# Optimization experiments

Measured on AMD Instinct MI355X. Metric: run time of the kernel, lower is better.

Reference implementation:

```python
import jax, jax.numpy as jnp
import numpy as np

D_MODEL = 256
NUM_HEADS = 8
CHUNK = 500
KEY_DIM = D_MODEL // NUM_HEADS      # 32
HEAD_DIM = KEY_DIM                  # value_factor = 1
SCALING = KEY_DIM ** -0.5
B, C, T = 2, 4, 2000                # T must be a multiple of CHUNK


def _rel_pos_constants(slen):
    # RetNetRelPos(chunkwise_recurrent=True)
    angle = 1.0 / (10000.0 ** jnp.linspace(0.0, 1.0, KEY_DIM // 2))
    angle = jnp.repeat(angle, 2)                                     # (KEY_DIM,)
    decay = jnp.log(1.0 - 2.0 ** (-5.0 - jnp.arange(NUM_HEADS, dtype=jnp.float32)))
    idx = jnp.arange(slen, dtype=jnp.float32)
    sin = jnp.sin(idx[:, None] * angle[None, :])                     # (T, KEY_DIM)
    cos = jnp.cos(idx[:, None] * angle[None, :])
    bi = jnp.arange(CHUNK, dtype=jnp.float32)
    diff = bi[:, None] - bi[None, :]
    mask = jnp.where(diff >= 0, jnp.exp(decay[:, None, None] * diff), 0.0)  # (H, cs, cs)
    last_row_sum = mask[:, -1].sum(-1)                               # (H,)
    value_inner_decay = (mask[:, -1] / last_row_sum[:, None])[:, :, None]   # (H, cs, 1)
    scale = jnp.sqrt(mask.sum(-1, keepdims=True))                    # (H, cs, 1)
    inner_mask = mask / scale
    cross_decay = jnp.exp(decay * CHUNK)[:, None, None]              # (H, 1, 1)
    qid = jnp.exp(decay[:, None] * (bi + 1.0))[:, :, None]           # (H, cs, 1)
    query_inner_decay = qid / (scale / last_row_sum[:, None, None])
    return sin, cos, inner_mask, cross_decay, query_inner_decay, value_inner_decay


def _rotate_every_two(x):
    x1, x2 = x[..., ::2], x[..., 1::2]
    return jnp.stack((-x2, x1), axis=-1).reshape(x.shape)


def _theta_shift(x, sin, cos):
    return x * cos + _rotate_every_two(x) * sin


def _layer_norm(x, g, b, eps=1e-5):
    mu = x.mean(-1, keepdims=True)
    var = ((x - mu) ** 2).mean(-1, keepdims=True)
    return (x - mu) * jax.lax.rsqrt(var + eps) * g + b


def _retention(x, qw, kw, vw, gw, ow):
    # MultiScaleRetention, chunkwise-recurrent mode
    bsz, t, _ = x.shape
    sin, cos, mask, cross_decay, q_decay, v_decay = _rel_pos_constants(t)
    q = x @ qw.T
    k = (x @ kw.T) * SCALING
    v = x @ vw.T
    g = x @ gw.T
    q = q.reshape(bsz, t, NUM_HEADS, KEY_DIM).transpose(0, 2, 1, 3)
    k = k.reshape(bsz, t, NUM_HEADS, KEY_DIM).transpose(0, 2, 1, 3)
    qr = _theta_shift(q, sin, cos)
    kr = _theta_shift(k, sin, cos)
    nc = t // CHUNK
    qr = qr.reshape(bsz, NUM_HEADS, nc, CHUNK, KEY_DIM).transpose(0, 2, 1, 3, 4)
    kr = kr.reshape(bsz, NUM_HEADS, nc, CHUNK, KEY_DIM).transpose(0, 2, 1, 3, 4)
    v = v.reshape(bsz, nc, CHUNK, NUM_HEADS, HEAD_DIM).transpose(0, 1, 3, 2, 4)
    qk = jnp.einsum('bnhik,bnhjk->bnhij', qr, kr) * mask             # (b,nc,h,cs,cs)
    inner_scale = jnp.maximum(jax.lax.stop_gradient(jnp.abs(qk)).sum(-1, keepdims=True), 1.0)
    inner_out = (qk / inner_scale) @ v                               # (b,nc,h,cs,hd)
    kv = jnp.einsum('bnhjk,bnhjd->bnhkd', kr, v * v_decay)           # (b,nc,h,kd,hd)

    def step(carry, kv_i):
        kv_state, kv_scale = carry
        out = (kv_state / kv_scale, kv_scale)
        kv_state = kv_state * cross_decay + kv_i
        kv_scale = jnp.maximum(
            jax.lax.stop_gradient(jnp.abs(kv_state)).sum(-2, keepdims=True).max(-1, keepdims=True), 1.0)
        return (kv_state, kv_scale), out

    init = (jnp.zeros((bsz, NUM_HEADS, KEY_DIM, HEAD_DIM), v.dtype),
            jnp.ones((bsz, NUM_HEADS, 1, 1), v.dtype))
    _, (kv_rec, cross_scale) = jax.lax.scan(step, init, jnp.moveaxis(kv, 1, 0))
    kv_rec = jnp.moveaxis(kv_rec, 0, 1)                              # (b,nc,h,kd,hd)
    cross_scale = jnp.moveaxis(cross_scale, 0, 1)                    # (b,nc,h,1,1)
    all_scale = jnp.maximum(inner_scale, cross_scale)
    cross_out = jnp.einsum('bnhik,bnhkd->bnhid', qr * q_decay, kv_rec)
    out = inner_out / (all_scale / inner_scale) + cross_out / (all_scale / cross_scale)
    out = out.transpose(0, 1, 3, 2, 4)                               # (b,nc,cs,h,hd)
    # group_norm = RMSNorm(head_dim, eps=1e-6, no affine)
    out = out * jax.lax.rsqrt(jnp.mean(out ** 2, -1, keepdims=True) + 1e-6)
    out = out.reshape(bsz, t, NUM_HEADS * HEAD_DIM)
    return (jax.nn.silu(g) * out) @ ow.T


def _mha(x, in_w, in_b, out_w, out_b):
    # torch.nn.MultiheadAttention, batch_first, eval (dropout off)
    bsz, s, _ = x.shape
    hd = D_MODEL // NUM_HEADS
    qkv = x @ in_w.T + in_b
    q, k, v = jnp.split(qkv, 3, axis=-1)
    q = q.reshape(bsz, s, NUM_HEADS, hd).transpose(0, 2, 1, 3) * (hd ** -0.5)
    k = k.reshape(bsz, s, NUM_HEADS, hd).transpose(0, 2, 1, 3)
    v = v.reshape(bsz, s, NUM_HEADS, hd).transpose(0, 2, 1, 3)
    attn = jax.nn.softmax(jnp.einsum('bhqd,bhkd->bhqk', q, k), axis=-1)
    out = jnp.einsum('bhqk,bhkd->bhqd', attn, v).transpose(0, 2, 1, 3).reshape(bsz, s, D_MODEL)
    return out @ out_w.T + out_b


def setup_inputs() -> dict:
    key = jax.random.key(0)
    ks = jax.random.split(key, 10)
    s = D_MODEL ** -0.5
    return {
        'inputs': jax.random.normal(ks[0], (B, C, T, D_MODEL), jnp.float32),
        'ln1_g': jnp.ones((D_MODEL,), jnp.float32),
        'ln1_b': jnp.zeros((D_MODEL,), jnp.float32),
        'ln2_g': jnp.ones((D_MODEL,), jnp.float32),
        'ln2_b': jnp.zeros((D_MODEL,), jnp.float32),
        'qw': jax.random.normal(ks[1], (D_MODEL, D_MODEL), jnp.float32) * s,
        'kw': jax.random.normal(ks[2], (D_MODEL, D_MODEL), jnp.float32) * s,
        'vw': jax.random.normal(ks[3], (D_MODEL, D_MODEL), jnp.float32) * s,
        'gw': jax.random.normal(ks[4], (D_MODEL, D_MODEL), jnp.float32) * s,
        'ow': jax.random.normal(ks[5], (D_MODEL, D_MODEL), jnp.float32) * s,
        'in_w': jax.random.normal(ks[6], (3 * D_MODEL, D_MODEL), jnp.float32) * s,
        'in_b': jnp.zeros((3 * D_MODEL,), jnp.float32),
        'out_w': jax.random.normal(ks[7], (D_MODEL, D_MODEL), jnp.float32) * s,
        'out_b': jnp.zeros((D_MODEL,), jnp.float32),
    }


def reference(inputs, ln1_g, ln1_b, ln2_g, ln2_b, qw, kw, vw, gw, ow, in_w, in_b, out_w, out_b):
    Bb, Cc, Tt, Dd = inputs.shape
    x = inputs.reshape(Bb * Cc, Tt, Dd)
    x = x + _retention(_layer_norm(x, ln1_g, ln1_b), qw, kw, vw, gw, ow)
    x = x.reshape(Bb, Cc, Tt, Dd).transpose(0, 2, 1, 3).reshape(Bb * Tt, Cc, Dd)
    x = x + _mha(_layer_norm(x, ln2_g, ln2_b), in_w, in_b, out_w, out_b)
    return x.reshape(Bb, Tt, Cc, Dd).transpose(0, 2, 1, 3)
```

## Files before the change

### kernel.cpp

```cpp
#include <hip/hip_runtime.h>
#include <math.h>

#define TLEN 2000
#define NSEQ 8
#define NHEADS 8
#define KD 32
#define CHUNKN 500
#define NCHUNK 4
#define MROWS 16000
#define SCALING 0.1767766952966369f

typedef float f32x4 __attribute__((ext_vector_type(4)));
typedef short s16x8 __attribute__((ext_vector_type(8)));
typedef unsigned short u16x8 __attribute__((ext_vector_type(8)));
typedef unsigned short u16x4 __attribute__((ext_vector_type(4)));

__device__ __forceinline__ unsigned short f2bf(float f) {
    unsigned int u = __float_as_uint(f);
    unsigned int r = (u + 0x7FFFu + ((u >> 16) & 1u)) >> 16;
    return (unsigned short)r;
}
__device__ __forceinline__ float bf2f(unsigned short h) {
    return __uint_as_float(((unsigned int)h) << 16);
}
__device__ __forceinline__ unsigned int cvtpk(float lo, float hi) {
    unsigned int r;
    asm("v_cvt_pk_bf16_f32 %0, %1, %2" : "=v"(r) : "v"(lo), "v"(hi));
    return r;
}

__global__ __launch_bounds__(256) void tab_kernel(float* __restrict__ sinT,
                                                  float* __restrict__ cosT) {
    int idx = blockIdx.x * 256 + threadIdx.x;
    if (idx >= TLEN * 16) return;
    int t = idx >> 4, a = idx & 15;
    float ang = powf(10000.0f, -(float)a / 15.0f);
    float th = (float)t * ang;
    sinT[idx] = sinf(th);
    cosT[idx] = cosf(th);
}

__global__ __launch_bounds__(256) void wcast_kernel(
    const float* __restrict__ qw, const float* __restrict__ kw,
    const float* __restrict__ vw, const float* __restrict__ gw,
    const float* __restrict__ ow, const float* __restrict__ inw,
    const float* __restrict__ outw, unsigned short* __restrict__ W) {
    int i = blockIdx.x * 1024 + threadIdx.x * 4;
    const float* src; int off;
    if (i < 65536)       { src = qw;   off = i; }
    else if (i < 131072) { src = kw;   off = i - 65536; }
    else if (i < 196608) { src = vw;   off = i - 131072; }
    else if (i < 262144) { src = gw;   off = i - 196608; }
    else if (i < 327680) { src = ow;   off = i - 262144; }
    else if (i < 524288) { src = inw;  off = i - 327680; }
    else                 { src = outw; off = i - 524288; }
    float4 v = *(const float4*)(src + off);
    u16x4 o;
    o[0] = f2bf(v.x); o[1] = f2bf(v.y); o[2] = f2bf(v.z); o[3] = f2bf(v.w);
    *(u16x4*)(W + i) = o;
}

__global__ __launch_bounds__(256) void ln_kernel(const float* __restrict__ x,
                                                 const float* __restrict__ gam,
                                                 const float* __restrict__ bet,
                                                 unsigned short* __restrict__ H,
                                                 unsigned short* __restrict__ L,
                                                 int rows) {
    int wid = threadIdx.x >> 6, lane = threadIdx.x & 63;
    int row = blockIdx.x * 4 + wid;
    if (row >= rows) return;
    const float* xr = x + (size_t)row * 256;
    float4 v = *(const float4*)(xr + lane * 4);
    float s = v.x + v.y + v.z + v.w;
    #pragma unroll
    for (int o = 32; o; o >>= 1) s += __shfl_xor(s, o);
    float mu = s * (1.0f / 256.0f);
    float dx = v.x - mu, dy = v.y - mu, dz = v.z - mu, dw = v.w - mu;
    float ss = dx * dx + dy * dy + dz * dz + dw * dw;
    #pragma unroll
    for (int o = 32; o; o >>= 1) ss += __shfl_xor(ss, o);
    float rstd = rsqrtf(ss * (1.0f / 256.0f) + 1e-5f);
    float4 g4 = *(const float4*)(gam + lane * 4);
    float4 b4 = *(const float4*)(bet + lane * 4);
    float ov[4];
    ov[0] = dx * rstd * g4.x + b4.x;
    ov[1] = dy * rstd * g4.y + b4.y;
    ov[2] = dz * rstd * g4.z + b4.z;
    ov[3] = dw * rstd * g4.w + b4.w;
    u16x4 hv, lv;
    #pragma unroll
    for (int j = 0; j < 4; ++j) {
        hv[j] = f2bf(ov[j]);
        lv[j] = f2bf(ov[j] - bf2f(hv[j]));
    }
    *(u16x4*)(H + (size_t)row * 256 + lane * 4) = hv;
    *(u16x4*)(L + (size_t)row * 256 + lane * 4) = lv;
}

template <int MODE>
__global__ __launch_bounds__(256, 2) void gemm_mfma(
    const unsigned short* __restrict__ AH, const unsigned short* __restrict__ AL,
    const unsigned short* __restrict__ Wc, const float* __restrict__ sinT,
    const float* __restrict__ cosT, const float* __restrict__ bias,
    const float* __restrict__ resid, float* __restrict__ F0,
    unsigned short* __restrict__ U0, unsigned short* __restrict__ U1,
    unsigned short* __restrict__ U2, unsigned short* __restrict__ U3,
    unsigned short* __restrict__ U4) {
    __shared__ unsigned short Ah[128][72];
    __shared__ unsigned short Al[128][72];
    __shared__ unsigned short Bt[128][72];
    const int tid = threadIdx.x;
    const int m0 = blockIdx.y * 128, n0 = blockIdx.x * 128;
    size_t wbase;
    if constexpr (MODE == 0)      wbase = (size_t)(n0 >> 8) * 65536 + (size_t)(n0 & 255) * 256;
    else if constexpr (MODE == 1) wbase = 262144 + (size_t)n0 * 256;
    else if constexpr (MODE == 2) wbase = 327680 + (size_t)n0 * 256;
    else                          wbase = 524288 + (size_t)n0 * 256;

    const int wid = tid >> 6, lane = tid & 63;
    const int wm = wid >> 1, wn = wid & 1;
    const int lr = lane & 15, lk = lane >> 4;
    const int str = tid >> 3;
    const int stc = (tid & 7) * 8;

    f32x4 acc[4][4] = {};

    for (int kt = 0; kt < 256; kt += 64) {
        if (kt) __syncthreads();
        #pragma unroll
        for (int it = 0; it < 4; ++it) {
            int r = it * 32 + str;
            u16x8 va = *(const u16x8*)(AH + (size_t)(m0 + r) * 256 + kt + stc);
            u16x8 vl = *(const u16x8*)(AL + (size_t)(m0 + r) * 256 + kt + stc);
            u16x8 vw = *(const u16x8*)(Wc + wbase + (size_t)r * 256 + kt + stc);
            *(u16x8*)(&Ah[r][stc]) = va;
            *(u16x8*)(&Al[r][stc]) = vl;
            *(u16x8*)(&Bt[r][stc]) = vw;
        }
        __syncthreads();
        #pragma unroll
        for (int ks = 0; ks < 2; ++ks) {
            const int k0 = ks * 32 + lk * 8;
            s16x8 af[4], alf[4], bf[4];
            #pragma unroll
            for (int f = 0; f < 4; ++f) {
                af[f]  = *(const s16x8*)(&Ah[wm * 64 + f * 16 + lr][k0]);
                alf[f] = *(const s16x8*)(&Al[wm * 64 + f * 16 + lr][k0]);
                bf[f]  = *(const s16x8*)(&Bt[wn * 64 + f * 16 + lr][k0]);
            }
            #pragma unroll
            for (int fm = 0; fm < 4; ++fm)
                #pragma unroll
                for (int fn = 0; fn < 4; ++fn) {
                    acc[fm][fn] = __builtin_amdgcn_mfma_f32_16x16x32_bf16(af[fm], bf[fn], acc[fm][fn], 0, 0, 0);
                    acc[fm][fn] = __builtin_amdgcn_mfma_f32_16x16x32_bf16(alf[fm], bf[fn], acc[fm][fn], 0, 0, 0);
                }
        }
    }

    if constexpr (MODE == 0) {
        const int w = n0 >> 8;
        if (w <= 1) {
            const float sc = (w == 1) ? SCALING : 1.0f;
            #pragma unroll
            for (int fn = 0; fn < 4; ++fn) {
                const int c = n0 + wn * 64 + fn * 16 + lr;
                const int d0 = c & 31;
                #pragma unroll
                for (int fm = 0; fm < 4; ++fm)
                    #pragma unroll
                    for (int r = 0; r < 4; ++r) {
                        const int i = m0 + wm * 64 + fm * 16 + lk * 4 + r;
                        const int t = i % TLEN;
                        float vraw = acc[fm][fn][r] * sc;
                        float oth = __shfl_xor(vraw, 1);
                        float cs = cosT[t * 16 + (d0 >> 1)];
                        float sn = sinT[t * 16 + (d0 >> 1)];
                        acc[fm][fn][r] = (d0 & 1) ? fmaf(vraw, cs, oth * sn)
                                                  : fmaf(vraw, cs, -(oth * sn));
                    }
            }
        }
        unsigned short* Dsel = (w == 0) ? U0 : (w == 1) ? U2 : (w == 2) ? U3 : U4;
        for (int half = 0; half < 2; ++half) {
            const int np = (w == 0) ? 2 : 1;
            for (int pass = 0; pass < np; ++pass) {
                __syncthreads();
                if (wn == half) {
                    #pragma unroll
                    for (int fn = 0; fn < 4; ++fn)
                        #pragma unroll
                        for (int fm = 0; fm < 4; ++fm)
                            #pragma unroll
                            for (int r = 0; r < 4; ++r) {
                                float x = acc[fm][fn][r];
                                unsigned short hb = f2bf(x);
                                unsigned short ob = pass ? f2bf(x - bf2f(hb)) : hb;
                                Ah[wm * 64 + fm * 16 + lk * 4 + r][fn * 16 + lr] = ob;
                            }
                }
                __syncthreads();
                unsigned short* D = (w == 0 && pass) ? U1 : Dsel;
                #pragma unroll
                for (int it = 0; it < 4; ++it) {
                    int flat = it * 2048 + tid * 8;
                    int r = flat >> 6, cl = flat & 63;
                    u16x8 val = *(const u16x8*)&Ah[r][cl];
                    int i = m0 + r;
                    int cb = (n0 & 255) + half * 64 + cl;
                    if (w <= 2) {
                        int bb = i / TLEN, t = i - bb * TLEN;
                        int hh = cb >> 5, d0 = cb & 31;
                        *(u16x8*)(D + ((size_t)(bb * NHEADS + hh) * TLEN + t) * KD + d0) = val;
                    } else {
                        *(u16x8*)(D + (size_t)i * 256 + cb) = val;
                    }
                }
            }
        }
    } else if constexpr (MODE == 1) {
        #pragma unroll
        for (int fn = 0; fn < 4; ++fn) {
            const int c = n0 + wn * 64 + fn * 16 + lr;
            #pragma unroll
            for (int fm = 0; fm < 4; ++fm)
                #pragma unroll
                for (int r = 0; r < 4; ++r) {
                    const int i = m0 + wm * 64 + fm * 16 + lk * 4 + r;
                    F0[(size_t)i * 256 + c] = resid[(size_t)i * 256 + c] + acc[fm][fn][r];
                }
        }
    } else if constexpr (MODE == 2) {
        const int w = n0 >> 8;
        const float qs = (w == 0) ? SCALING : 1.0f;
        unsigned short* Dsel = (w == 0) ? U0 : (w == 1) ? U1 : U2;
        #pragma unroll
        for (int fn = 0; fn < 4; ++fn) {
            const int c = n0 + wn * 64 + fn * 16 + lr;
            const float bv = bias[c];
            #pragma unroll
            for (int fm = 0; fm < 4; ++fm)
                #pragma unroll
                for (int r = 0; r < 4; ++r)
                    acc[fm][fn][r] = (acc[fm][fn][r] + bv) * qs;
        }
        for (int half = 0; half < 2; ++half) {
            __syncthreads();
            if (wn == half) {
                #pragma unroll
                for (int fn = 0; fn < 4; ++fn)
                    #pragma unroll
                    for (int fm = 0; fm < 4; ++fm)
                        #pragma unroll
                        for (int r = 0; r < 4; ++r)
                            Ah[wm * 64 + fm * 16 + lk * 4 + r][fn * 16 + lr] =
                                f2bf(acc[fm][fn][r]);
            }
            __syncthreads();
            #pragma unroll
            for (int it = 0; it < 4; ++it) {
                int flat = it * 2048 + tid * 8;
                int r = flat >> 6, cl = flat & 63;
                u16x8 val = *(const u16x8*)&Ah[r][cl];
                int i = m0 + r;
                int cb = (n0 & 255) + half * 64 + cl;
                *(u16x8*)(Dsel + (size_t)i * 256 + cb) = val;
            }
        }
    } else {
        #pragma unroll
        for (int fn = 0; fn < 4; ++fn) {
            const int c = n0 + wn * 64 + fn * 16 + lr;
            const float bv = bias[c];
            #pragma unroll
            for (int fm = 0; fm < 4; ++fm)
                #pragma unroll
                for (int r = 0; r < 4; ++r) {
                    const int i = m0 + wm * 64 + fm * 16 + lk * 4 + r;
                    F0[(size_t)i * 256 + c] = resid[(size_t)i * 256 + c] + acc[fm][fn][r] + bv;
                }
        }
    }
}

__global__ __launch_bounds__(256) void kvp_kernel(const unsigned short* __restrict__ KB,
                                                  const unsigned short* __restrict__ VB,
                                                  float* __restrict__ kvp) {
    int blk = blockIdx.x;
    int sub = blk & 1, rest = blk >> 1;
    int b = rest >> 5, n = (rest >> 3) & 3, h = rest & 7;
    int tid = threadIdx.x;
    int k = tid >> 3, d0 = (tid & 7) * 4;
    float dec = logf(1.0f - exp2f(-5.0f - (float)h));
    float lrs = (1.0f - expf(dec * (float)CHUNKN)) / (1.0f - expf(dec));
    float invl = 1.0f / lrs;
    const unsigned short* krb = KB + ((size_t)(b * NHEADS + h) * TLEN + n * CHUNKN) * KD;
    const unsigned short* vb = VB + ((size_t)(b * NHEADS + h) * TLEN + n * CHUNKN) * KD;
    float a0 = 0, a1 = 0, a2 = 0, a3 = 0;
    int j0 = sub * 250;
    for (int j = j0; j < j0 + 250; ++j) {
        float kj = bf2f(krb[(size_t)j * KD + k]);
        float vd = expf(dec * (float)(CHUNKN - 1 - j)) * invl;
        float w = kj * vd;
        u16x4 vv = *(const u16x4*)(vb + (size_t)j * KD + d0);
        a0 = fmaf(w, bf2f(vv[0]), a0); a1 = fmaf(w, bf2f(vv[1]), a1);
        a2 = fmaf(w, bf2f(vv[2]), a2); a3 = fmaf(w, bf2f(vv[3]), a3);
    }
    float* dst = kvp + ((size_t)rest * 2 + sub) * 1024 + k * 32 + d0;
    dst[0] = a0; dst[1] = a1; dst[2] = a2; dst[3] = a3;
}

__global__ __launch_bounds__(256) void scan_kernel(const float* __restrict__ kvp,
                                                   float* __restrict__ rec,
                                                   float* __restrict__ sig) {
    __shared__ float cs[32];
    __shared__ float ssig;
    int blk = blockIdx.x;
    int b = blk >> 3, h = blk & 7;
    int tid = threadIdx.x;
    float dec = logf(1.0f - exp2f(-5.0f - (float)h));
    float cd = expf(dec * (float)CHUNKN);
    float S0 = 0, S1 = 0, S2 = 0, S3 = 0;
    float sigma = 1.0f;
    for (int n = 0; n < NCHUNK; ++n) {
        int rest = b * 32 + n * 8 + h;
        size_t rbase = (size_t)rest * 1024;
        size_t pbase = (size_t)rest * 2048;
        rec[rbase + tid] = S0;
        rec[rbase + tid + 256] = S1;
        rec[rbase + tid + 512] = S2;
        rec[rbase + tid + 768] = S3;
        if (tid == 0) sig[rest] = sigma;
        float k0 = 0, k1 = 0, k2 = 0, k3 = 0;
        #pragma unroll
        for (int s = 0; s < 2; ++s) {
            k0 += kvp[pbase + s * 1024 + tid];
            k1 += kvp[pbase + s * 1024 + tid + 256];
            k2 += kvp[pbase + s * 1024 + tid + 512];
            k3 += kvp[pbase + s * 1024 + tid + 768];
        }
        S0 = S0 * cd + k0;
        S1 = S1 * cd + k1;
        S2 = S2 * cd + k2;
        S3 = S3 * cd + k3;
        if (tid < 32) cs[tid] = 0.f;
        __syncthreads();
        float part = fabsf(S0) + fabsf(S1) + fabsf(S2) + fabsf(S3);
        atomicAdd(&cs[tid & 31], part);
        __syncthreads();
        if (tid == 0) {
            float m = cs[0];
            for (int d = 1; d < 32; ++d) m = fmaxf(m, cs[d]);
            ssig = fmaxf(m, 1.0f);
        }
        __syncthreads();
        sigma = ssig;
    }
}

__global__ __launch_bounds__(256, 2) void ret_core3(
    const unsigned short* __restrict__ QH, const unsigned short* __restrict__ QL,
    const unsigned short* __restrict__ KB, const unsigned short* __restrict__ VB,
    const unsigned short* __restrict__ GB,
    const float* __restrict__ rec, const float* __restrict__ sig,
    unsigned short* __restrict__ ABH, unsigned short* __restrict__ ABL) {
    __shared__ unsigned short Kt[64][40];
    __shared__ unsigned short Vt[32][72];
    __shared__ unsigned short SpH[32][40];
    __shared__ unsigned short SpL[32][40];
    __shared__ unsigned short Pl[128][72];

    const int u = 3 - (int)(blockIdx.x >> 8);
    const int chunk = blockIdx.x & 255;
    const int b = chunk >> 5, n = (chunk >> 3) & 3, h = chunk & 7;
    const int tid = threadIdx.x;
    const int wid = tid >> 6, lane = tid & 63;
    const int c = lane & 15, gq = lane >> 4;
    const float dec = logf(1.0f - exp2f(-5.0f - (float)h));
    const float ndec = -dec;
    const size_t cb16 = ((size_t)(b * NHEADS + h) * TLEN + n * CHUNKN) * KD;
    const int i0 = u * 128 + wid * 32;
    const int NT = 2 * u + 2;
    const int jtmax_w = (i0 + 31) >> 6;

    s16x8 qh[2], ql[2];
    #pragma unroll
    for (int fi = 0; fi < 2; ++fi) {
        size_t off = cb16 + (size_t)(i0 + fi * 16 + c) * KD + gq * 8;
        qh[fi] = *(const s16x8*)(QH + off);
        ql[fi] = *(const s16x8*)(QL + off);
    }

    {
        int e0 = tid * 4;
        int k = e0 >> 5, d0 = e0 & 31;
        float4 sv = *(const float4*)(rec + (size_t)chunk * 1024 + e0);
        float se[4] = {sv.x, sv.y, sv.z, sv.w};
        #pragma unroll
        for (int j = 0; j < 4; ++j) {
            unsigned short hb = f2bf(se[j]);
            SpH[d0 + j][k] = hb;
            SpL[d0 + j][k] = f2bf(se[j] - bf2f(hb));
        }
    }

    f32x4 ot[2][2] = {};
    float absI[2] = {0.f, 0.f};

    for (int jt = 0; jt < NT; ++jt) {
        if (jt) __syncthreads();
        {
            int jl = tid >> 2, d0 = (tid & 3) * 8;
            int jg = jt * 64 + jl;
            float ej = expf(ndec * (float)jg);
            u16x8 kraw = *(const u16x8*)(KB + cb16 + (size_t)jg * KD + d0);
            u16x8 vraw = *(const u16x8*)(VB + cb16 + (size_t)jg * KD + d0);
            u16x8 kb;
            #pragma unroll
            for (int e = 0; e < 8; ++e) kb[e] = f2bf(bf2f(kraw[e]) * ej);
            *(u16x8*)&Kt[jl][d0] = kb;
            #pragma unroll
            for (int e = 0; e < 8; ++e) Vt[d0 + e][jl] = vraw[e];
        }
        __syncthreads();
        if (jt <= jtmax_w) {
            f32x4 st[4][2] = {};
            s16x8 ka[4];
            #pragma unroll
            for (int jf = 0; jf < 4; ++jf)
                ka[jf] = *(const s16x8*)&Kt[jf * 16 + c][gq * 8];
            #pragma unroll
            for (int jf = 0; jf < 4; ++jf)
                #pragma unroll
                for (int fi = 0; fi < 2; ++fi) {
                    st[jf][fi] = __builtin_amdgcn_mfma_f32_16x16x32_bf16(ka[jf], qh[fi], st[jf][fi], 0, 0, 0);
                    st[jf][fi] = __builtin_amdgcn_mfma_f32_16x16x32_bf16(ka[jf], ql[fi], st[jf][fi], 0, 0, 0);
                }
            const bool domask = (jt * 64 + 63 > i0);
            #pragma unroll
            for (int jf = 0; jf < 4; ++jf)
                #pragma unroll
                for (int fi = 0; fi < 2; ++fi) {
                    const int ii = i0 + fi * 16 + c;
                    if (domask) {
                        #pragma unroll
                        for (int r = 0; r < 4; ++r) {
                            int jg = jt * 64 + jf * 16 + gq * 4 + r;
                            if (jg > ii) st[jf][fi][r] = 0.f;
                        }
                    }
                    absI[fi] += (fabsf(st[jf][fi][0]) + fabsf(st[jf][fi][1])) +
                                (fabsf(st[jf][fi][2]) + fabsf(st[jf][fi][3]));
                    uint2 pw;
                    pw.x = cvtpk(st[jf][fi][0], st[jf][fi][1]);
                    pw.y = cvtpk(st[jf][fi][2], st[jf][fi][3]);
                    *(uint2*)&Pl[wid * 32 + fi * 16 + c][jf * 16 + gq * 4] = pw;
                }
            #pragma unroll
            for (int js = 0; js < 2; ++js) {
                s16x8 va0 = *(const s16x8*)&Vt[c][js * 32 + gq * 8];
                s16x8 va1 = *(const s16x8*)&Vt[16 + c][js * 32 + gq * 8];
                #pragma unroll
                for (int fi = 0; fi < 2; ++fi) {
                    s16x8 pb = *(const s16x8*)&Pl[wid * 32 + fi * 16 + c][js * 32 + gq * 8];
                    ot[0][fi] = __builtin_amdgcn_mfma_f32_16x16x32_bf16(va0, pb, ot[0][fi], 0, 0, 0);
                    ot[1][fi] = __builtin_amdgcn_mfma_f32_16x16x32_bf16(va1, pb, ot[1][fi], 0, 0, 0);
                }
            }
        }
    }

    f32x4 xt[2][2] = {};
    #pragma unroll
    for (int fd = 0; fd < 2; ++fd) {
        s16x8 sh = *(const s16x8*)&SpH[fd * 16 + c][gq * 8];
        s16x8 sl = *(const s16x8*)&SpL[fd * 16 + c][gq * 8];
        #pragma unroll
        for (int fi = 0; fi < 2; ++fi) {
            xt[fd][fi] = __builtin_amdgcn_mfma_f32_16x16x32_bf16(sh, qh[fi], xt[fd][fi], 0, 0, 0);
            xt[fd][fi] = __builtin_amdgcn_mfma_f32_16x16x32_bf16(sh, ql[fi], xt[fd][fi], 0, 0, 0);
            xt[fd][fi] = __builtin_amdgcn_mfma_f32_16x16x32_bf16(sl, qh[fi], xt[fd][fi], 0, 0, 0);
        }
    }

    const float er = expf(dec);
    const float inv1mr = 1.0f / (1.0f - er);
    const float lrs = (1.0f - expf(dec * (float)CHUNKN)) * inv1mr;
    const float sgp = sig[chunk];
    #pragma unroll
    for (int fi = 0; fi < 2; ++fi) {
        absI[fi] += __shfl_xor(absI[fi], 16);
        absI[fi] += __shfl_xor(absI[fi], 32);
        const int ii = i0 + fi * 16 + c;
        float rowsum = (1.0f - expf(dec * (float)(ii + 1))) * inv1mr;
        float iscale = rsqrtf(rowsum);
        float f_i = expf(dec * (float)ii) * iscale;
        float inner = fmaxf(absI[fi] * f_i, 1.0f);
        float alls = fmaxf(inner, sgp);
        float qd = expf(dec * (float)(ii + 1)) * lrs * iscale;
        float inva = 1.0f / alls;
        float vals[2][4];
        float ms = 0.f;
        #pragma unroll
        for (int fd = 0; fd < 2; ++fd)
            #pragma unroll
            for (int r = 0; r < 4; ++r) {
                float t = (ot[fd][fi][r] * f_i + xt[fd][fi][r] * qd) * inva;
                vals[fd][r] = t;
                ms += t * t;
            }
        ms += __shfl_xor(ms, 16);
        ms += __shfl_xor(ms, 32);
        float rn = rsqrtf(ms * (1.0f / 32.0f) + 1e-6f);
        const int tg = n * CHUNKN + ii;
        const unsigned short* gp = GB + ((size_t)b * TLEN + tg) * 256 + h * KD;
        #pragma unroll
        for (int fd = 0; fd < 2; ++fd) {
            u16x4 gv = *(const u16x4*)(gp + fd * 16 + gq * 4);
            unsigned short hb[4], lb[4];
            #pragma unroll
            for (int r = 0; r < 4; ++r) {
                float ge = bf2f(gv[r]);
                float sg = ge / (1.0f + expf(-ge));
                float ov = sg * vals[fd][r] * rn;
                hb[r] = f2bf(ov);
                lb[r] = f2bf(ov - bf2f(hb[r]));
            }
            uint2 ph, plw;
            ph.x = (unsigned int)hb[0] | ((unsigned int)hb[1] << 16);
            ph.y = (unsigned int)hb[2] | ((unsigned int)hb[3] << 16);
            plw.x = (unsigned int)lb[0] | ((unsigned int)lb[1] << 16);
            plw.y = (unsigned int)lb[2] | ((unsigned int)lb[3] << 16);
            *(uint2*)&Pl[wid * 32 + fi * 16 + c][fd * 16 + gq * 4] = ph;
            *(uint2*)&Pl[wid * 32 + fi * 16 + c][36 + fd * 16 + gq * 4] = plw;
        }
    }
    __syncthreads();
    {
        int r = tid & 127, half = tid >> 7;
        int ig = u * 128 + r;
        if (ig < CHUNKN) {
            unsigned short* D = half ? ABL : ABH;
            size_t dst = ((size_t)b * TLEN + n * CHUNKN + ig) * 256 + h * KD;
            #pragma unroll
            for (int k = 0; k < 4; ++k) {
                u16x4 a = *(const u16x4*)&Pl[r][half * 36 + k * 8];
                u16x4 bq = *(const u16x4*)&Pl[r][half * 36 + k * 8 + 4];
                u16x8 w;
                w[0] = a[0]; w[1] = a[1]; w[2] = a[2]; w[3] = a[3];
                w[4] = bq[0]; w[5] = bq[1]; w[6] = bq[2]; w[7] = bq[3];
                *(u16x8*)(D + dst + k * 8) = w;
            }
        }
    }
}

__global__ __launch_bounds__(256) void mha_attn(const unsigned short* __restrict__ qh_,
                                                const unsigned short* __restrict__ kh_,
                                                const unsigned short* __restrict__ vh_,
                                                unsigned short* __restrict__ OH,
                                                unsigned short* __restrict__ OL) {
    int gidx = blockIdx.x * 256 + threadIdx.x;
    if (gidx >= 2 * TLEN * NHEADS * 4) return;
    int i = gidx & 3;
    int h = (gidx >> 2) & 7;
    int rest = gidx >> 5;
    int t = rest % TLEN;
    int b = rest / TLEN;
    size_t rows[4];
    #pragma unroll
    for (int c = 0; c < 4; ++c) rows[c] = ((size_t)(b * 4 + c) * TLEN + t);
    float q[32];
    #pragma unroll
    for (int rb = 0; rb < 4; ++rb) {
        u16x8 t8 = *(const u16x8*)(qh_ + rows[i] * 256 + h * 32 + rb * 8);
        #pragma unroll
        for (int e = 0; e < 8; ++e) q[rb * 8 + e] = bf2f(t8[e]);
    }
    float s[4];
    #pragma unroll
    for (int j = 0; j < 4; ++j) {
        const unsigned short* kp = kh_ + rows[j] * 256 + h * 32;
        float a0 = 0, a1 = 0, a2 = 0, a3 = 0;
        #pragma unroll
        for (int rb = 0; rb < 4; ++rb) {
            u16x8 t8 = *(const u16x8*)(kp + rb * 8);
            a0 = fmaf(q[rb * 8 + 0], bf2f(t8[0]), a0);
            a1 = fmaf(q[rb * 8 + 1], bf2f(t8[1]), a1);
            a2 = fmaf(q[rb * 8 + 2], bf2f(t8[2]), a2);
            a3 = fmaf(q[rb * 8 + 3], bf2f(t8[3]), a3);
            a0 = fmaf(q[rb * 8 + 4], bf2f(t8[4]), a0);
            a1 = fmaf(q[rb * 8 + 5], bf2f(t8[5]), a1);
            a2 = fmaf(q[rb * 8 + 6], bf2f(t8[6]), a2);
            a3 = fmaf(q[rb * 8 + 7], bf2f(t8[7]), a3);
        }
        s[j] = (a0 + a1) + (a2 + a3);
    }
    float m = fmaxf(fmaxf(s[0], s[1]), fmaxf(s[2], s[3]));
    float p[4], den = 0.f;
    #pragma unroll
    for (int j = 0; j < 4; ++j) { p[j] = expf(s[j] - m); den += p[j]; }
    float inv = 1.0f / den;
    float o[32];
    #pragma unroll
    for (int e = 0; e < 32; ++e) o[e] = 0.f;
    #pragma unroll
    for (int j = 0; j < 4; ++j) {
        float wj = p[j] * inv;
        const unsigned short* vp = vh_ + rows[j] * 256 + h * 32;
        #pragma unroll
        for (int rb = 0; rb < 4; ++rb) {
            u16x8 t8 = *(const u16x8*)(vp + rb * 8);
            #pragma unroll
            for (int e = 0; e < 8; ++e)
                o[rb * 8 + e] = fmaf(wj, bf2f(t8[e]), o[rb * 8 + e]);
        }
    }
    #pragma unroll
    for (int rb = 0; rb < 8; ++rb) {
        u16x4 hv, lv;
        #pragma unroll
        for (int e = 0; e < 4; ++e) {
            float x = o[rb * 4 + e];
            hv[e] = f2bf(x);
            lv[e] = f2bf(x - bf2f(hv[e]));
        }
        *(u16x4*)(OH + rows[i] * 256 + h * 32 + rb * 4) = hv;
        *(u16x4*)(OL + rows[i] * 256 + h * 32 + rb * 4) = lv;
    }
}

extern "C" void kernel_launch(void* const* d_in, const int* in_sizes, int n_in,
                              void* d_out, int out_size, void* d_ws, size_t ws_size,
                              hipStream_t stream) {
    (void)in_sizes; (void)n_in; (void)out_size; (void)ws_size;
    const float* x    = (const float*)d_in[0];
    const float* ln1g = (const float*)d_in[1];
    const float* ln1b = (const float*)d_in[2];
    const float* ln2g = (const float*)d_in[3];
    const float* ln2b = (const float*)d_in[4];
    const float* qw   = (const float*)d_in[5];
    const float* kw   = (const float*)d_in[6];
    const float* vw   = (const float*)d_in[7];
    const float* gw   = (const float*)d_in[8];
    const float* ow   = (const float*)d_in[9];
    const float* in_w = (const float*)d_in[10];
    const float* in_b = (const float*)d_in[11];
    const float* outw = (const float*)d_in[12];
    const float* outb = (const float*)d_in[13];
    float* out = (float*)d_out;
    float* ws = (float*)d_ws;

    constexpr size_t O_SIN = 0;
    constexpr size_t O_COS = 32000;
    constexpr size_t O_W   = 64000;
    constexpr size_t O_QH  = 358912;
    constexpr size_t O_QL  = O_QH + 2048000;
    constexpr size_t O_KB  = O_QL + 2048000;
    constexpr size_t O_VB  = O_KB + 2048000;
    constexpr size_t O_GB  = O_VB + 2048000;
    constexpr size_t O_H   = O_GB + 2048000;
    constexpr size_t O_L   = O_H + 2048000;
    constexpr size_t O_REC = O_L + 2048000;
    constexpr size_t O_SIG = O_REC + 262144;

    float* sinT = ws + O_SIN;
    float* cosT = ws + O_COS;
    unsigned short* Wc = (unsigned short*)(ws + O_W);
    unsigned short* QH = (unsigned short*)(ws + O_QH);
    unsigned short* QL = (unsigned short*)(ws + O_QL);
    unsigned short* KB = (unsigned short*)(ws + O_KB);
    unsigned short* VB = (unsigned short*)(ws + O_VB);
    unsigned short* GB = (unsigned short*)(ws + O_GB);
    unsigned short* H  = (unsigned short*)(ws + O_H);
    unsigned short* L  = (unsigned short*)(ws + O_L);
    float* x2   = ws + O_QH;
    unsigned short* qhat = KB;
    unsigned short* khat = VB;
    unsigned short* vhat = GB;
    float* kvpf = ws + O_H;
    float* recb = ws + O_REC;
    float* sigb = ws + O_SIG;

    tab_kernel<<<125, 256, 0, stream>>>(sinT, cosT);
    wcast_kernel<<<576, 256, 0, stream>>>(qw, kw, vw, gw, ow, in_w, outw, Wc);
    ln_kernel<<<MROWS / 4, 256, 0, stream>>>(x, ln1g, ln1b, H, L, MROWS);
    gemm_mfma<0><<<dim3(8, 125), 256, 0, stream>>>(H, L, Wc, sinT, cosT, nullptr,
                                                   nullptr, nullptr, QH, QL, KB, VB, GB);
    kvp_kernel<<<512, 256, 0, stream>>>(KB, VB, kvpf);
    scan_kernel<<<64, 256, 0, stream>>>(kvpf, recb, sigb);
    ret_core3<<<1024, 256, 0, stream>>>(QH, QL, KB, VB, GB, recb, sigb, H, L);
    gemm_mfma<1><<<dim3(2, 125), 256, 0, stream>>>(H, L, Wc, nullptr, nullptr,
                                                   nullptr, x, x2,
                                                   nullptr, nullptr, nullptr, nullptr, nullptr);
    ln_kernel<<<MROWS / 4, 256, 0, stream>>>(x2, ln2g, ln2b, H, L, MROWS);
    gemm_mfma<2><<<dim3(6, 125), 256, 0, stream>>>(H, L, Wc, nullptr, nullptr,
                                                   in_b, nullptr, nullptr,
                                                   qhat, khat, vhat, nullptr, nullptr);
    mha_attn<<<500, 256, 0, stream>>>(qhat, khat, vhat, H, L);
    gemm_mfma<3><<<dim3(2, 125), 256, 0, stream>>>(H, L, Wc, nullptr, nullptr,
                                                   outb, x2, out,
                                                   nullptr, nullptr, nullptr, nullptr, nullptr);
}
```

Measured before the change: 271.1 us.

## Load GEMM MFMA fragments directly from global memory, dropping LDS staging

The GEMM main loop no longer stages A-high, A-low and weight tiles through shared memory with barriers. Each wave now reads its MFMA operand fragments straight from global memory, over a fully unrolled K loop. Shared memory shrinks to a single tile used only by the epilogue, and launch bounds rise to allow three blocks per CU. This removes the LDS round-trip and syncs, but gives up reuse between waves, so each wave re-reads A and W from global/L2 with 16-byte per-lane strided loads.

After: 352.3 us. +30.0%, slower.

```diff
diff --git a/kernel.cpp b/kernel.cpp
--- a/kernel.cpp
+++ b/kernel.cpp
@@ -98,7 +98,7 @@
 }
 
 template <int MODE>
-__global__ __launch_bounds__(256, 2) void gemm_mfma(
+__global__ __launch_bounds__(256, 3) void gemm_mfma(
     const unsigned short* __restrict__ AH, const unsigned short* __restrict__ AL,
     const unsigned short* __restrict__ Wc, const float* __restrict__ sinT,
     const float* __restrict__ cosT, const float* __restrict__ bias,
@@ -106,9 +106,7 @@
     unsigned short* __restrict__ U0, unsigned short* __restrict__ U1,
     unsigned short* __restrict__ U2, unsigned short* __restrict__ U3,
     unsigned short* __restrict__ U4) {
-    __shared__ unsigned short Ah[128][72];
-    __shared__ unsigned short Al[128][72];
-    __shared__ unsigned short Bt[128][72];
+    __shared__ unsigned short St[128][72];
     const int tid = threadIdx.x;
     const int m0 = blockIdx.y * 128, n0 = blockIdx.x * 128;
     size_t wbase;
@@ -120,44 +118,33 @@
     const int wid = tid >> 6, lane = tid & 63;
     const int wm = wid >> 1, wn = wid & 1;
     const int lr = lane & 15, lk = lane >> 4;
-    const int str = tid >> 3;
-    const int stc = (tid & 7) * 8;
+
+    const unsigned short* Ab = AH + (size_t)(m0 + wm * 64 + lr) * 256 + lk * 8;
+    const unsigned short* Lb = AL + (size_t)(m0 + wm * 64 + lr) * 256 + lk * 8;
+    const unsigned short* Wb = Wc + wbase + (size_t)(wn * 64 + lr) * 256 + lk * 8;
 
     f32x4 acc[4][4] = {};
 
-    for (int kt = 0; kt < 256; kt += 64) {
-        if (kt) __syncthreads();
-        #pragma unroll
-        for (int it = 0; it < 4; ++it) {
-            int r = it * 32 + str;
-            u16x8 va = *(const u16x8*)(AH + (size_t)(m0 + r) * 256 + kt + stc);
-            u16x8 vl = *(const u16x8*)(AL + (size_t)(m0 + r) * 256 + kt + stc);
-            u16x8 vw = *(const u16x8*)(Wc + wbase + (size_t)r * 256 + kt + stc);
-            *(u16x8*)(&Ah[r][stc]) = va;
-            *(u16x8*)(&Al[r][stc]) = vl;
-            *(u16x8*)(&Bt[r][stc]) = vw;
-        }
-        __syncthreads();
-        #pragma unroll
-        for (int ks = 0; ks < 2; ++ks) {
-            const int k0 = ks * 32 + lk * 8;
-            s16x8 af[4], alf[4], bf[4];
-            #pragma unroll
-            for (int f = 0; f < 4; ++f) {
-                af[f]  = *(const s16x8*)(&Ah[wm * 64 + f * 16 + lr][k0]);
-                alf[f] = *(const s16x8*)(&Al[wm * 64 + f * 16 + lr][k0]);
-                bf[f]  = *(const s16x8*)(&Bt[wn * 64 + f * 16 + lr][k0]);
-            }
-            #pragma unroll
-            for (int fm = 0; fm < 4; ++fm)
-                #pragma unroll
-                for (int fn = 0; fn < 4; ++fn) {
-                    acc[fm][fn] = __builtin_amdgcn_mfma_f32_16x16x32_bf16(af[fm], bf[fn], acc[fm][fn], 0, 0, 0);
-                    acc[fm][fn] = __builtin_amdgcn_mfma_f32_16x16x32_bf16(alf[fm], bf[fn], acc[fm][fn], 0, 0, 0);
-                }
-        }
-    }
-
+    #pragma unroll
+    for (int kk = 0; kk < 8; ++kk) {
+        const int kof = kk * 32;
+        s16x8 af[4], alf[4], bf[4];
+        #pragma unroll
+        for (int f = 0; f < 4; ++f) {
+            af[f]  = *(const s16x8*)(Ab + (size_t)f * 4096 + kof);
+            alf[f] = *(const s16x8*)(Lb + (size_t)f * 4096 + kof);
+            bf[f]  = *(const s16x8*)(Wb + (size_t)f * 4096 + kof);
+        }
+        #pragma unroll
+        for (int fm = 0; fm < 4; ++fm)
+            #pragma unroll
+            for (int fn = 0; fn < 4; ++fn) {
+                acc[fm][fn] = __builtin_amdgcn_mfma_f32_16x16x32_bf16(af[fm], bf[fn], acc[fm][fn], 0, 0, 0);
+                acc[fm][fn] = __builtin_amdgcn_mfma_f32_16x16x32_bf16(alf[fm], bf[fn], acc[fm][fn], 0, 0, 0);
+            }
+    }
+
+    const int lk4 = lk;
     if constexpr (MODE == 0) {
         const int w = n0 >> 8;
         if (w <= 1) {
@@ -170,7 +157,7 @@
                 for (int fm = 0; fm < 4; ++fm)
                     #pragma unroll
                     for (int r = 0; r < 4; ++r) {
-                        const int i = m0 + wm * 64 + fm * 16 + lk * 4 + r;
+                        const int i = m0 + wm * 64 + fm * 16 + lk4 * 4 + r;
                         const int t = i % TLEN;
                         float vraw = acc[fm][fn][r] * sc;
                         float oth = __shfl_xor(vraw, 1);
@@ -196,7 +183,7 @@
                                 float x = acc[fm][fn][r];
                                 unsigned short hb = f2bf(x);
                                 unsigned short ob = pass ? f2bf(x - bf2f(hb)) : hb;
-                                Ah[wm * 64 + fm * 16 + lk * 4 + r][fn * 16 + lr] = ob;
+                                St[wm * 64 + fm * 16 + lk4 * 4 + r][fn * 16 + lr] = ob;
                             }
                 }
                 __syncthreads();
@@ -205,7 +192,7 @@
                 for (int it = 0; it < 4; ++it) {
                     int flat = it * 2048 + tid * 8;
                     int r = flat >> 6, cl = flat & 63;
-                    u16x8 val = *(const u16x8*)&Ah[r][cl];
+                    u16x8 val = *(const u16x8*)&St[r][cl];
                     int i = m0 + r;
                     int cb = (n0 & 255) + half * 64 + cl;
                     if (w <= 2) {
@@ -226,7 +213,7 @@
             for (int fm = 0; fm < 4; ++fm)
                 #pragma unroll
                 for (int r = 0; r < 4; ++r) {
-                    const int i = m0 + wm * 64 + fm * 16 + lk * 4 + r;
+                    const int i = m0 + wm * 64 + fm * 16 + lk4 * 4 + r;
                     F0[(size_t)i * 256 + c] = resid[(size_t)i * 256 + c] + acc[fm][fn][r];
                 }
         }
@@ -253,7 +240,7 @@
                     for (int fm = 0; fm < 4; ++fm)
                         #pragma unroll
                         for (int r = 0; r < 4; ++r)
-                            Ah[wm * 64 + fm * 16 + lk * 4 + r][fn * 16 + lr] =
+                            St[wm * 64 + fm * 16 + lk4 * 4 + r][fn * 16 + lr] =
                                 f2bf(acc[fm][fn][r]);
             }
             __syncthreads();
@@ -261,7 +248,7 @@
             for (int it = 0; it < 4; ++it) {
                 int flat = it * 2048 + tid * 8;
                 int r = flat >> 6, cl = flat & 63;
-                u16x8 val = *(const u16x8*)&Ah[r][cl];
+                u16x8 val = *(const u16x8*)&St[r][cl];
                 int i = m0 + r;
                 int cb = (n0 & 255) + half * 64 + cl;
                 *(u16x8*)(Dsel + (size_t)i * 256 + cb) = val;
@@ -276,7 +263,7 @@
             for (int fm = 0; fm < 4; ++fm)
                 #pragma unroll
                 for (int r = 0; r < 4; ++r) {
-                    const int i = m0 + wm * 64 + fm * 16 + lk * 4 + r;
+                    const int i = m0 + wm * 64 + fm * 16 + lk4 * 4 + r;
                     F0[(size_t)i * 256 + c] = resid[(size_t)i * 256 + c] + acc[fm][fn][r] + bv;
                 }
         }
```
